# Optimization experiments

Hardware: AMD Instinct MI355X
Metric: run time of the kernel (lower is better)

Reference implementation:

```python
import jax, jax.numpy as jnp
import numpy as np

N_IN = 500000
C = 64
K = 27          # kernel volume 3^3
P = 150000      # max pairs per kernel offset
NUM_OUT = 200000


def setup_inputs() -> dict:
    key = jax.random.key(0)
    k1, k2, k3 = jax.random.split(key, 3)
    features = jax.random.normal(k1, (N_IN, C), dtype=jnp.float32)
    # indice_pairs[k, 0, :] = input voxel indices, indice_pairs[k, 1, :] = output voxel indices
    indice_pairs = jax.random.randint(k2, (K, 2, P), 0, NUM_OUT, dtype=jnp.int32)
    indice_pairs_num = jax.random.randint(k3, (K,), 0, P, dtype=jnp.int32)
    return {
        "features": features,
        "indice_pairs": indice_pairs,
        "indice_pairs_num": indice_pairs_num,
        "num_out": NUM_OUT,
    }


def reference(features, indice_pairs, indice_pairs_num, num_out):
    """spconv-style indice_avgpool: gather -> scatter-sum -> divide by count."""
    Kk, _, Pp = indice_pairs.shape
    in_idx = indice_pairs[:, 0, :]   # [K, P]
    out_idx = indice_pairs[:, 1, :]  # [K, P]
    # pairs beyond indice_pairs_num[k] are padding and must be ignored
    valid = jnp.arange(Pp, dtype=jnp.int32)[None, :] < indice_pairs_num[:, None]  # [K, P]
    vmask = valid.astype(features.dtype)
    gathered = features[in_idx.reshape(-1)] * vmask.reshape(-1, 1)               # [K*P, C]
    out_flat = jnp.where(valid, out_idx, 0).reshape(-1)                           # safe scatter target
    out_sum = jnp.zeros((num_out, features.shape[1]), features.dtype).at[out_flat].add(gathered)
    counts = jnp.zeros((num_out,), features.dtype).at[out_flat].add(vmask.reshape(-1))
    return out_sum / jnp.maximum(counts, 1.0)[:, None]
```

## Files before the change

kernel.cpp:

```cpp
#include <hip/hip_runtime.h>

constexpr int N_IN    = 500000;
constexpr int C       = 64;
constexpr int K       = 27;
constexpr int P       = 150000;
constexpr int NUM_OUT = 200000;
constexpr int TOTAL_PAIRS = K * P;
constexpr int OUT_ELEMS   = NUM_OUT * C;

constexpr int OUT_PER_BIN = 128;
constexpr int BIN_SHIFT   = 7;
constexpr int NBINS       = (NUM_OUT + OUT_PER_BIN - 1) / OUT_PER_BIN;

constexpr int PPB        = 16384;
constexpr int PART_BLKS  = (TOTAL_PAIRS + PPB - 1) / PPB;

constexpr int CAP  = 2560;

constexpr int HOUT   = 64;
constexpr int CAPC_H = 1536;

#define PACK(o_local, in) (((unsigned)(o_local) << 18) | (unsigned)(in))

__global__ void __launch_bounds__(1024)
ap_partition(const int* __restrict__ pairs, const int* __restrict__ nums,
             int* __restrict__ cursor, unsigned int* __restrict__ appendBuf)
{
    __shared__ int binCnt[NBINS];
    __shared__ int binOff[NBINS];
    __shared__ int binDst[NBINS];
    __shared__ int scanTmp[1024];
    __shared__ int snums[K];
    __shared__ unsigned int stage[PPB];
    __shared__ unsigned short sbin[PPB];

    const int tid = threadIdx.x;
    for (int i = tid; i < NBINS; i += 1024) binCnt[i] = 0;
    if (tid < K) snums[tid] = nums[tid];
    __syncthreads();

    const int gbase = blockIdx.x * PPB;

    int4 oc[4];
    int  kk[4];
    int  pp[4];
    int  vv[4];
    #pragma unroll
    for (int j = 0; j < 4; ++j) {
        const int g0 = gbase + (j * 1024 + tid) * 4;
        int v = 0;
        if (g0 < TOTAL_PAIRS) {
            const int k = g0 / P;
            const int p0 = g0 - k * P;
            const int n = snums[k];
            v = n - p0;
            v = v < 0 ? 0 : (v > 4 ? 4 : v);
            kk[j] = k; pp[j] = p0;
            if (v > 0) {
                const int4 o4 = *(const int4*)&pairs[(k * 2 + 1) * P + p0];
                oc[j] = o4;
                atomicAdd(&binCnt[o4.x >> BIN_SHIFT], 1);
                if (v > 1) atomicAdd(&binCnt[o4.y >> BIN_SHIFT], 1);
                if (v > 2) atomicAdd(&binCnt[o4.z >> BIN_SHIFT], 1);
                if (v > 3) atomicAdd(&binCnt[o4.w >> BIN_SHIFT], 1);
            }
        }
        vv[j] = v;
    }
    __syncthreads();

    const int b0 = 2 * tid, b1 = 2 * tid + 1;
    const int c0 = (b0 < NBINS) ? binCnt[b0] : 0;
    const int c1 = (b1 < NBINS) ? binCnt[b1] : 0;
    scanTmp[tid] = c0 + c1;
    __syncthreads();
    for (int d = 1; d < 1024; d <<= 1) {
        int x = (tid >= d) ? scanTmp[tid - d] : 0;
        __syncthreads();
        scanTmp[tid] += x;
        __syncthreads();
    }
    const int Eblk = scanTmp[1023];
    const int ex = scanTmp[tid] - (c0 + c1);
    if (b0 < NBINS) {
        binOff[b0] = ex;
        if (c0 > 0) {
            const int g = atomicAdd(&cursor[b0], c0);
            binDst[b0] = b0 * CAP + g - ex;
        }
        binCnt[b0] = 0;
    }
    if (b1 < NBINS) {
        binOff[b1] = ex + c0;
        if (c1 > 0) {
            const int g = atomicAdd(&cursor[b1], c1);
            binDst[b1] = b1 * CAP + g - (ex + c0);
        }
        binCnt[b1] = 0;
    }
    __syncthreads();

    #pragma unroll
    for (int j = 0; j < 4; ++j) {
        const int v = vv[j];
        if (v > 0) {
            const int4 o4 = oc[j];
            const int4 i4 = *(const int4*)&pairs[(kk[j] * 2) * P + pp[j]];
            {
                const int b = o4.x >> BIN_SHIFT;
                const int pos = binOff[b] + atomicAdd(&binCnt[b], 1);
                stage[pos] = PACK(o4.x & (OUT_PER_BIN - 1), i4.x);
                sbin[pos] = (unsigned short)b;
            }
            if (v > 1) {
                const int b = o4.y >> BIN_SHIFT;
                const int pos = binOff[b] + atomicAdd(&binCnt[b], 1);
                stage[pos] = PACK(o4.y & (OUT_PER_BIN - 1), i4.y);
                sbin[pos] = (unsigned short)b;
            }
            if (v > 2) {
                const int b = o4.z >> BIN_SHIFT;
                const int pos = binOff[b] + atomicAdd(&binCnt[b], 1);
                stage[pos] = PACK(o4.z & (OUT_PER_BIN - 1), i4.z);
                sbin[pos] = (unsigned short)b;
            }
            if (v > 3) {
                const int b = o4.w >> BIN_SHIFT;
                const int pos = binOff[b] + atomicAdd(&binCnt[b], 1);
                stage[pos] = PACK(o4.w & (OUT_PER_BIN - 1), i4.w);
                sbin[pos] = (unsigned short)b;
            }
        }
    }
    __syncthreads();

    for (int e = tid; e < Eblk; e += 1024) {
        const int bb = sbin[e];
        const int d = binDst[bb] + e;
        if (d - bb * CAP < CAP) appendBuf[d] = stage[e];
    }
}

__global__ void __launch_bounds__(128, 8)
ap_bin_reduce(const float* __restrict__ features,
              const unsigned int* __restrict__ appendBuf,
              const int* __restrict__ cursor,
              float* __restrict__ out)
{
    __shared__ int hist[HOUT];
    __shared__ int sc[HOUT];
    __shared__ int cur[HOUT];
    __shared__ unsigned int lb[CAPC_H];

    const int tid  = threadIdx.x;
    const int b    = blockIdx.x >> 1;
    const int half = blockIdx.x & 1;
    const int segBase = b * CAP;
    const int Eb   = min(cursor[b], CAP);
    const int obase = b * OUT_PER_BIN + half * HOUT;

    if (tid < HOUT) hist[tid] = 0;
    __syncthreads();

    uint4 ew[5];
    #pragma unroll
    for (int j = 0; j < 5; ++j) {
        const int e0 = (j * 128 + tid) * 4;
        uint4 w = make_uint4(~0u, ~0u, ~0u, ~0u);
        if (e0 < Eb) {
            w = *(const uint4*)&appendBuf[segBase + e0];
            if (e0 + 1 >= Eb) w.y = ~0u;
            if (e0 + 2 >= Eb) w.z = ~0u;
            if (e0 + 3 >= Eb) w.w = ~0u;
            if (w.x != ~0u) {
                if (((w.x >> 24) & 1) == (unsigned)half)
                    atomicAdd(&hist[(w.x >> 18) & 63], 1);
                else w.x = ~0u;
            }
            if (w.y != ~0u) {
                if (((w.y >> 24) & 1) == (unsigned)half)
                    atomicAdd(&hist[(w.y >> 18) & 63], 1);
                else w.y = ~0u;
            }
            if (w.z != ~0u) {
                if (((w.z >> 24) & 1) == (unsigned)half)
                    atomicAdd(&hist[(w.z >> 18) & 63], 1);
                else w.z = ~0u;
            }
            if (w.w != ~0u) {
                if (((w.w >> 24) & 1) == (unsigned)half)
                    atomicAdd(&hist[(w.w >> 18) & 63], 1);
                else w.w = ~0u;
            }
        }
        ew[j] = w;
    }
    __syncthreads();

    int myc = 0;
    if (tid < HOUT) { myc = hist[tid]; sc[tid] = myc; }
    __syncthreads();
    #pragma unroll
    for (int d = 1; d < HOUT; d <<= 1) {
        int x = 0;
        if (tid < HOUT && tid >= d) x = sc[tid - d];
        __syncthreads();
        if (tid < HOUT) sc[tid] += x;
        __syncthreads();
    }
    if (tid < HOUT) cur[tid] = sc[tid] - myc;
    __syncthreads();

    #pragma unroll
    for (int j = 0; j < 5; ++j) {
        const uint4 w = ew[j];
        if (w.x != ~0u) { const int p = atomicAdd(&cur[(w.x >> 18) & 63], 1);
                          if (p < CAPC_H) lb[p] = w.x & 0x3FFFFu; }
        if (w.y != ~0u) { const int p = atomicAdd(&cur[(w.y >> 18) & 63], 1);
                          if (p < CAPC_H) lb[p] = w.y & 0x3FFFFu; }
        if (w.z != ~0u) { const int p = atomicAdd(&cur[(w.z >> 18) & 63], 1);
                          if (p < CAPC_H) lb[p] = w.z & 0x3FFFFu; }
        if (w.w != ~0u) { const int p = atomicAdd(&cur[(w.w >> 18) & 63], 1);
                          if (p < CAPC_H) lb[p] = w.w & 0x3FFFFu; }
    }
    __syncthreads();

    const int qq = tid >> 4;
    const int cl = tid & 15;
    const float* fbase = features + cl * 4;

    for (int r = 0; r < 4; ++r) {
        const int olA = qq * 8 + r;
        const int olB = olA + 4;
        const int oA = obase + olA;
        const int oB = obase + olB;
        const int numA = hist[olA];
        const int numB = hist[olB];
        int sA = min(cur[olA] - numA, CAPC_H);
        int sB = min(cur[olB] - numB, CAPC_H);
        const int mA = min(sA + numA, CAPC_H) - sA;
        const int mB = min(sB + numB, CAPC_H) - sB;

        float4 a = make_float4(0.f, 0.f, 0.f, 0.f);
        float4 c = make_float4(0.f, 0.f, 0.f, 0.f);
        int eA = 0, eB = 0;

        while (eA + 4 <= mA && eB + 4 <= mB) {
            const int iA0 = (int)lb[sA + eA + 0];
            const int iA1 = (int)lb[sA + eA + 1];
            const int iA2 = (int)lb[sA + eA + 2];
            const int iA3 = (int)lb[sA + eA + 3];
            const int iB0 = (int)lb[sB + eB + 0];
            const int iB1 = (int)lb[sB + eB + 1];
            const int iB2 = (int)lb[sB + eB + 2];
            const int iB3 = (int)lb[sB + eB + 3];
            const float4 vA0 = *(const float4*)&fbase[(size_t)iA0 * C];
            const float4 vA1 = *(const float4*)&fbase[(size_t)iA1 * C];
            const float4 vA2 = *(const float4*)&fbase[(size_t)iA2 * C];
            const float4 vA3 = *(const float4*)&fbase[(size_t)iA3 * C];
            const float4 vB0 = *(const float4*)&fbase[(size_t)iB0 * C];
            const float4 vB1 = *(const float4*)&fbase[(size_t)iB1 * C];
            const float4 vB2 = *(const float4*)&fbase[(size_t)iB2 * C];
            const float4 vB3 = *(const float4*)&fbase[(size_t)iB3 * C];
            a.x += (vA0.x + vA1.x) + (vA2.x + vA3.x);
            a.y += (vA0.y + vA1.y) + (vA2.y + vA3.y);
            a.z += (vA0.z + vA1.z) + (vA2.z + vA3.z);
            a.w += (vA0.w + vA1.w) + (vA2.w + vA3.w);
            c.x += (vB0.x + vB1.x) + (vB2.x + vB3.x);
            c.y += (vB0.y + vB1.y) + (vB2.y + vB3.y);
            c.z += (vB0.z + vB1.z) + (vB2.z + vB3.z);
            c.w += (vB0.w + vB1.w) + (vB2.w + vB3.w);
            eA += 4; eB += 4;
        }
        for (; eA + 4 <= mA; eA += 4) {
            const int i0 = (int)lb[sA + eA + 0];
            const int i1 = (int)lb[sA + eA + 1];
            const int i2 = (int)lb[sA + eA + 2];
            const int i3 = (int)lb[sA + eA + 3];
            const float4 v0 = *(const float4*)&fbase[(size_t)i0 * C];
            const float4 v1 = *(const float4*)&fbase[(size_t)i1 * C];
            const float4 v2 = *(const float4*)&fbase[(size_t)i2 * C];
            const float4 v3 = *(const float4*)&fbase[(size_t)i3 * C];
            a.x += (v0.x + v1.x) + (v2.x + v3.x);
            a.y += (v0.y + v1.y) + (v2.y + v3.y);
            a.z += (v0.z + v1.z) + (v2.z + v3.z);
            a.w += (v0.w + v1.w) + (v2.w + v3.w);
        }
        for (; eA < mA; ++eA) {
            const int i0 = (int)lb[sA + eA];
            const float4 v0 = *(const float4*)&fbase[(size_t)i0 * C];
            a.x += v0.x; a.y += v0.y; a.z += v0.z; a.w += v0.w;
        }
        for (; eB + 4 <= mB; eB += 4) {
            const int i0 = (int)lb[sB + eB + 0];
            const int i1 = (int)lb[sB + eB + 1];
            const int i2 = (int)lb[sB + eB + 2];
            const int i3 = (int)lb[sB + eB + 3];
            const float4 v0 = *(const float4*)&fbase[(size_t)i0 * C];
            const float4 v1 = *(const float4*)&fbase[(size_t)i1 * C];
            const float4 v2 = *(const float4*)&fbase[(size_t)i2 * C];
            const float4 v3 = *(const float4*)&fbase[(size_t)i3 * C];
            c.x += (v0.x + v1.x) + (v2.x + v3.x);
            c.y += (v0.y + v1.y) + (v2.y + v3.y);
            c.z += (v0.z + v1.z) + (v2.z + v3.z);
            c.w += (v0.w + v1.w) + (v2.w + v3.w);
        }
        for (; eB < mB; ++eB) {
            const int i0 = (int)lb[sB + eB];
            const float4 v0 = *(const float4*)&fbase[(size_t)i0 * C];
            c.x += v0.x; c.y += v0.y; c.z += v0.z; c.w += v0.w;
        }

        if (oA < NUM_OUT) {
            const float inv = 1.0f / fmaxf((float)numA, 1.0f);
            a.x *= inv; a.y *= inv; a.z *= inv; a.w *= inv;
            *(float4*)&out[(size_t)oA * C + cl * 4] = a;
        }
        if (oB < NUM_OUT) {
            const float inv = 1.0f / fmaxf((float)numB, 1.0f);
            c.x *= inv; c.y *= inv; c.z *= inv; c.w *= inv;
            *(float4*)&out[(size_t)oB * C + cl * 4] = c;
        }
    }
}

__global__ void __launch_bounds__(256)
sparse_avgpool_scatter(const float* __restrict__ features,
                       const int*   __restrict__ pairs,
                       const int*   __restrict__ nums,
                       float*       __restrict__ out_sum,
                       int*         __restrict__ counts)
{
    const int lane = threadIdx.x & 63;
    const int g = blockIdx.x * (blockDim.x >> 6) + (threadIdx.x >> 6);
    if (g >= TOTAL_PAIRS) return;
    const int k = g / P;
    const int p = g - k * P;
    if (p >= nums[k]) return;
    const int in_idx  = pairs[(k * 2    ) * P + p];
    const int out_idx = pairs[(k * 2 + 1) * P + p];
    const float v = features[(size_t)in_idx * C + lane];
    atomicAdd(&out_sum[(size_t)out_idx * C + lane], v);
    if (lane == 0) atomicAdd(&counts[out_idx], 1);
}

__global__ void __launch_bounds__(256)
sparse_avgpool_divide(float* __restrict__ out, const int* __restrict__ counts)
{
    const int i = blockIdx.x * blockDim.x + threadIdx.x;
    if (i >= OUT_ELEMS) return;
    out[i] /= fmaxf((float)counts[i >> 6], 1.0f);
}

extern "C" void kernel_launch(void* const* d_in, const int* in_sizes, int n_in,
                              void* d_out, int out_size, void* d_ws, size_t ws_size,
                              hipStream_t stream)
{
    const float* features = (const float*)d_in[0];
    const int*   pairs    = (const int*)d_in[1];
    const int*   nums     = (const int*)d_in[2];
    float* out = (float*)d_out;

    const size_t need = (size_t)(2048 + (size_t)NBINS * CAP) * sizeof(int) + 64;

    if (ws_size < need) {
        float* out_sum = out;
        int* counts = (int*)d_ws;
        hipMemsetAsync(out_sum, 0, (size_t)OUT_ELEMS * sizeof(float), stream);
        hipMemsetAsync(counts, 0, (size_t)NUM_OUT * sizeof(int), stream);
        sparse_avgpool_scatter<<<(TOTAL_PAIRS + 3) / 4, 256, 0, stream>>>(
            features, pairs, nums, out, counts);
        sparse_avgpool_divide<<<(OUT_ELEMS + 255) / 256, 256, 0, stream>>>(
            out, counts);
        return;
    }

    int* cursor = (int*)d_ws;
    unsigned int* appendBuf = (unsigned int*)(cursor + 2048);

    hipMemsetAsync(cursor, 0, 2048 * sizeof(int), stream);

    ap_partition<<<PART_BLKS, 1024, 0, stream>>>(pairs, nums, cursor, appendBuf);
    ap_bin_reduce<<<NBINS * 2, 128, 0, stream>>>(features, appendBuf, cursor, out);
}
```

Baseline: 274.2 us.

## Replace shared-memory block binning with direct global atomic append per pair

```diff
diff --git a/kernel.cpp b/kernel.cpp
--- a/kernel.cpp
+++ b/kernel.cpp
@@ -12,9 +12,6 @@
 constexpr int BIN_SHIFT   = 7;
 constexpr int NBINS       = (NUM_OUT + OUT_PER_BIN - 1) / OUT_PER_BIN;
 
-constexpr int PPB        = 16384;
-constexpr int PART_BLKS  = (TOTAL_PAIRS + PPB - 1) / PPB;
-
 constexpr int CAP  = 2560;
 
 constexpr int HOUT   = 64;
@@ -22,122 +19,45 @@
 
 #define PACK(o_local, in) (((unsigned)(o_local) << 18) | (unsigned)(in))
 
-__global__ void __launch_bounds__(1024)
+__global__ void __launch_bounds__(256)
 ap_partition(const int* __restrict__ pairs, const int* __restrict__ nums,
              int* __restrict__ cursor, unsigned int* __restrict__ appendBuf)
 {
-    __shared__ int binCnt[NBINS];
-    __shared__ int binOff[NBINS];
-    __shared__ int binDst[NBINS];
-    __shared__ int scanTmp[1024];
-    __shared__ int snums[K];
-    __shared__ unsigned int stage[PPB];
-    __shared__ unsigned short sbin[PPB];
-
-    const int tid = threadIdx.x;
-    for (int i = tid; i < NBINS; i += 1024) binCnt[i] = 0;
-    if (tid < K) snums[tid] = nums[tid];
-    __syncthreads();
-
-    const int gbase = blockIdx.x * PPB;
-
-    int4 oc[4];
-    int  kk[4];
-    int  pp[4];
-    int  vv[4];
-    #pragma unroll
-    for (int j = 0; j < 4; ++j) {
-        const int g0 = gbase + (j * 1024 + tid) * 4;
-        int v = 0;
-        if (g0 < TOTAL_PAIRS) {
-            const int k = g0 / P;
-            const int p0 = g0 - k * P;
-            const int n = snums[k];
-            v = n - p0;
-            v = v < 0 ? 0 : (v > 4 ? 4 : v);
-            kk[j] = k; pp[j] = p0;
-            if (v > 0) {
-                const int4 o4 = *(const int4*)&pairs[(k * 2 + 1) * P + p0];
-                oc[j] = o4;
-                atomicAdd(&binCnt[o4.x >> BIN_SHIFT], 1);
-                if (v > 1) atomicAdd(&binCnt[o4.y >> BIN_SHIFT], 1);
-                if (v > 2) atomicAdd(&binCnt[o4.z >> BIN_SHIFT], 1);
-                if (v > 3) atomicAdd(&binCnt[o4.w >> BIN_SHIFT], 1);
-            }
-        }
-        vv[j] = v;
-    }
-    __syncthreads();
-
-    const int b0 = 2 * tid, b1 = 2 * tid + 1;
-    const int c0 = (b0 < NBINS) ? binCnt[b0] : 0;
-    const int c1 = (b1 < NBINS) ? binCnt[b1] : 0;
-    scanTmp[tid] = c0 + c1;
-    __syncthreads();
-    for (int d = 1; d < 1024; d <<= 1) {
-        int x = (tid >= d) ? scanTmp[tid - d] : 0;
-        __syncthreads();
-        scanTmp[tid] += x;
-        __syncthreads();
-    }
-    const int Eblk = scanTmp[1023];
-    const int ex = scanTmp[tid] - (c0 + c1);
-    if (b0 < NBINS) {
-        binOff[b0] = ex;
-        if (c0 > 0) {
-            const int g = atomicAdd(&cursor[b0], c0);
-            binDst[b0] = b0 * CAP + g - ex;
-        }
-        binCnt[b0] = 0;
-    }
-    if (b1 < NBINS) {
-        binOff[b1] = ex + c0;
-        if (c1 > 0) {
-            const int g = atomicAdd(&cursor[b1], c1);
-            binDst[b1] = b1 * CAP + g - (ex + c0);
-        }
-        binCnt[b1] = 0;
-    }
-    __syncthreads();
-
-    #pragma unroll
-    for (int j = 0; j < 4; ++j) {
-        const int v = vv[j];
-        if (v > 0) {
-            const int4 o4 = oc[j];
-            const int4 i4 = *(const int4*)&pairs[(kk[j] * 2) * P + pp[j]];
-            {
-                const int b = o4.x >> BIN_SHIFT;
-                const int pos = binOff[b] + atomicAdd(&binCnt[b], 1);
-                stage[pos] = PACK(o4.x & (OUT_PER_BIN - 1), i4.x);
-                sbin[pos] = (unsigned short)b;
-            }
-            if (v > 1) {
-                const int b = o4.y >> BIN_SHIFT;
-                const int pos = binOff[b] + atomicAdd(&binCnt[b], 1);
-                stage[pos] = PACK(o4.y & (OUT_PER_BIN - 1), i4.y);
-                sbin[pos] = (unsigned short)b;
-            }
-            if (v > 2) {
-                const int b = o4.z >> BIN_SHIFT;
-                const int pos = binOff[b] + atomicAdd(&binCnt[b], 1);
-                stage[pos] = PACK(o4.z & (OUT_PER_BIN - 1), i4.z);
-                sbin[pos] = (unsigned short)b;
-            }
-            if (v > 3) {
-                const int b = o4.w >> BIN_SHIFT;
-                const int pos = binOff[b] + atomicAdd(&binCnt[b], 1);
-                stage[pos] = PACK(o4.w & (OUT_PER_BIN - 1), i4.w);
-                sbin[pos] = (unsigned short)b;
-            }
-        }
-    }
-    __syncthreads();
-
-    for (int e = tid; e < Eblk; e += 1024) {
-        const int bb = sbin[e];
-        const int d = binDst[bb] + e;
-        if (d - bb * CAP < CAP) appendBuf[d] = stage[e];
+    const int t0 = blockIdx.x * 256 + threadIdx.x;
+    const int nthr = gridDim.x * 256;
+
+    for (int q = t0; q < TOTAL_PAIRS / 4; q += nthr) {
+        const int g0 = q * 4;
+        const int k  = g0 / P;
+        const int p0 = g0 - k * P;
+        const int n  = nums[k];
+        int v = n - p0;
+        v = v < 0 ? 0 : (v > 4 ? 4 : v);
+        if (v <= 0) continue;
+
+        const int4 o4 = *(const int4*)&pairs[(k * 2 + 1) * P + p0];
+        const int4 i4 = *(const int4*)&pairs[(k * 2    ) * P + p0];
+
+        {
+            const int b = o4.x >> BIN_SHIFT;
+            const int s = atomicAdd(&cursor[b], 1);
+            if (s < CAP) appendBuf[b * CAP + s] = PACK(o4.x & (OUT_PER_BIN - 1), i4.x);
+        }
+        if (v > 1) {
+            const int b = o4.y >> BIN_SHIFT;
+            const int s = atomicAdd(&cursor[b], 1);
+            if (s < CAP) appendBuf[b * CAP + s] = PACK(o4.y & (OUT_PER_BIN - 1), i4.y);
+        }
+        if (v > 2) {
+            const int b = o4.z >> BIN_SHIFT;
+            const int s = atomicAdd(&cursor[b], 1);
+            if (s < CAP) appendBuf[b * CAP + s] = PACK(o4.z & (OUT_PER_BIN - 1), i4.z);
+        }
+        if (v > 3) {
+            const int b = o4.w >> BIN_SHIFT;
+            const int s = atomicAdd(&cursor[b], 1);
+            if (s < CAP) appendBuf[b * CAP + s] = PACK(o4.w & (OUT_PER_BIN - 1), i4.w);
+        }
     }
 }
 
@@ -380,6 +300,6 @@
 
     hipMemsetAsync(cursor, 0, 2048 * sizeof(int), stream);
 
-    ap_partition<<<PART_BLKS, 1024, 0, stream>>>(pairs, nums, cursor, appendBuf);
+    ap_partition<<<2048, 256, 0, stream>>>(pairs, nums, cursor, appendBuf);
     ap_bin_reduce<<<NBINS * 2, 128, 0, stream>>>(features, appendBuf, cursor, out);
 }
```

Result: slower. 533.5 us (+94.6%).
